# Performance work log

Hardware: AMD Instinct MI355X
Metric: run time of the kernel (lower is better)

Reference implementation:

```python
import jax, jax.numpy as jnp
import numpy as np

B, T, C, H = 4, 4096, 2048, 128  # batch, seq, emb_dim, head_size


def setup_inputs() -> dict:
    key = jax.random.key(0)
    k1, k2, k3, k4 = jax.random.split(key, 4)
    idx = jax.random.normal(k1, (B, T, C), dtype=jnp.float32)
    # nn.Linear weight layout: [out_features, in_features]; scale like torch init
    s = 1.0 / np.sqrt(C)
    Wq = jax.random.uniform(k2, (H, C), jnp.float32, -s, s)
    Wk = jax.random.uniform(k3, (H, C), jnp.float32, -s, s)
    Wv = jax.random.uniform(k4, (H, C), jnp.float32, -s, s)
    return {"idx": idx, "Wq": Wq, "Wk": Wk, "Wv": Wv}


def reference(idx, Wq, Wk, Wv):
    b, t, c = idx.shape
    q = jnp.einsum('btc,hc->bth', idx, Wq)  # [B,T,H]
    k = jnp.einsum('btc,hc->bth', idx, Wk)
    v = jnp.einsum('btc,hc->bth', idx, Wv)
    # NOTE: original computes keys @ queries^T and scales by emb_dim**-0.5
    scale = jnp.asarray(c, idx.dtype) ** -0.5
    wei = jnp.einsum('bih,bjh->bij', k, q) * scale  # [B,T,T]
    causal = jnp.tril(jnp.ones((t, t), dtype=bool))
    wei = jnp.where(causal, wei, -jnp.inf)
    wei = jax.nn.softmax(wei, axis=-1)
    return jnp.einsum('bij,bjh->bih', wei, v)  # [B,T,H]
```

## Files before the change

kernel.cpp:

```cpp
#include <hip/hip_runtime.h>
#include <hip/hip_bf16.h>
#include <cstdint>

#define TSEQ 4096
#define CDIM 2048
#define HDIM 128

typedef short bf8v __attribute__((ext_vector_type(8)));
typedef float f4v  __attribute__((ext_vector_type(4)));

__device__ __forceinline__ unsigned short f2b(float f) {
  union { float f; unsigned u; } v; v.f = f;
  unsigned u = v.u;
  return (unsigned short)((u + 0x7fffu + ((u >> 16) & 1u)) >> 16);
}

__device__ __forceinline__ f4v mfma16(bf8v a, bf8v b, f4v c) {
  return __builtin_amdgcn_mfma_f32_16x16x32_bf16(a, b, c, 0, 0, 0);
}

__global__ void wcat_kernel(const float* __restrict__ Wq, const float* __restrict__ Wk,
                            const float* __restrict__ Wv, unsigned short* __restrict__ Wcat) {
  int e = (blockIdx.x * 256 + threadIdx.x) * 4;
  int n = e >> 11;
  int k = e & 2047;
  const float* src;
  if (n < 128)      src = Wq + (size_t)n * CDIM + k;
  else if (n < 256) src = Wk + (size_t)(n - 128) * CDIM + k;
  else              src = Wv + (size_t)(n - 256) * CDIM + k;
  float4 f = *(const float4*)src;
  ushort4 o;
  o.x = f2b(f.x); o.y = f2b(f.y); o.z = f2b(f.z); o.w = f2b(f.w);
  *(ushort4*)(Wcat + e) = o;
}

__global__ __launch_bounds__(512, 6) void proj_gemm(const float* __restrict__ A,
                                                    const unsigned short* __restrict__ Bw,
                                                    unsigned short* __restrict__ QB,
                                                    unsigned short* __restrict__ KA,
                                                    unsigned short* __restrict__ VB) {
  __shared__ union {
    struct { unsigned short As[2][64][40]; unsigned short Bs[2][128][40]; } st;
    unsigned short Ct[64][132];
  } sm;
  const int m0 = blockIdx.x * 64;
  const int y  = blockIdx.y;
  const int n0 = y * 128;
  const int tid = threadIdx.x;
  const int lane = tid & 63;
  const int w = tid >> 6;
  const int wm = (w & 1) * 32, wn = (w >> 1) * 32;
  const int llo = lane & 15, lhi = lane >> 4;

  f4v acc[2][2];
#pragma unroll
  for (int i = 0; i < 2; ++i)
#pragma unroll
    for (int j = 0; j < 2; ++j) acc[i][j] = (f4v){0.f, 0.f, 0.f, 0.f};

  const int arow = tid >> 3, acol = (tid & 7) * 4;
  const int brow = tid >> 2, bcol = (tid & 3) * 8;
  const float* aptr = A + (size_t)(m0 + arow) * CDIM + acol;
  const unsigned short* bptr = Bw + (size_t)(n0 + brow) * CDIM + bcol;

  float4 fa = *(const float4*)(aptr);
  uint4  ub = *(const uint4*)(bptr);
  {
    ushort4 o;
    o.x = f2b(fa.x); o.y = f2b(fa.y); o.z = f2b(fa.z); o.w = f2b(fa.w);
    *(ushort4*)&sm.st.As[0][arow][acol] = o;
    *(uint4*)&sm.st.Bs[0][brow][bcol]   = ub;
  }

  for (int it = 0; it < 64; ++it) {
    const int cur = it & 1;
    __syncthreads();
    if (it < 63) {
      fa = *(const float4*)(aptr + (it + 1) * 32);
      ub = *(const uint4*)(bptr + (it + 1) * 32);
    }
    bf8v af[2], bfr[2];
    af[0]  = *(const bf8v*)&sm.st.As[cur][wm + llo][lhi * 8];
    af[1]  = *(const bf8v*)&sm.st.As[cur][wm + 16 + llo][lhi * 8];
    bfr[0] = *(const bf8v*)&sm.st.Bs[cur][wn + llo][lhi * 8];
    bfr[1] = *(const bf8v*)&sm.st.Bs[cur][wn + 16 + llo][lhi * 8];
#pragma unroll
    for (int i = 0; i < 2; ++i)
#pragma unroll
      for (int j = 0; j < 2; ++j) acc[i][j] = mfma16(af[i], bfr[j], acc[i][j]);
    if (it < 63) {
      ushort4 o;
      o.x = f2b(fa.x); o.y = f2b(fa.y); o.z = f2b(fa.z); o.w = f2b(fa.w);
      int nxt = cur ^ 1;
      *(ushort4*)&sm.st.As[nxt][arow][acol] = o;
      *(uint4*)&sm.st.Bs[nxt][brow][bcol]   = ub;
    }
  }
  __syncthreads();
#pragma unroll
  for (int i = 0; i < 2; ++i)
#pragma unroll
    for (int j = 0; j < 2; ++j)
#pragma unroll
      for (int r = 0; r < 4; ++r)
        sm.Ct[wm + i * 16 + lhi * 4 + r][wn + j * 16 + llo] = f2b(acc[i][j][r]);
  __syncthreads();
  if (y < 2) {
    unsigned short* dst = (y == 0) ? QB : KA;
    const size_t base16 = (size_t)(m0 >> 4);
#pragma unroll
    for (int p = 0; p < 2; ++p) {
      int g = p * 512 + tid;
      int t16l = g >> 8, kk = (g >> 6) & 3, ln = g & 63;
      int lo = ln & 15, hi = ln >> 4;
      bf8v v = *(const bf8v*)&sm.Ct[t16l * 16 + lo][kk * 32 + hi * 8];
      *(bf8v*)(dst + (((base16 + t16l) * 4 + kk) * 64 + ln) * 8) = v;
    }
  } else {
    const size_t base32 = (size_t)(m0 >> 5);
#pragma unroll
    for (int p = 0; p < 3; ++p) {
      int g = p * 512 + tid;
      if (g < 1152) {
        int jbl = g / 576;
        int ht  = (g % 576) >> 6;
        int ln  = g & 63;
        int lo = ln & 15, hi = ln >> 4;
        bf8v v;
        if (ht == 8) {
#pragma unroll
          for (int e = 0; e < 8; ++e) v[e] = (lo == 0) ? (short)0x3F80 : (short)0;
        } else {
#pragma unroll
          for (int e = 0; e < 8; ++e) v[e] = (short)sm.Ct[jbl * 32 + hi * 8 + e][ht * 16 + lo];
        }
        *(bf8v*)(VB + (((base32 + jbl) * 9 + ht) * 512 + (size_t)ln * 8)) = v;
      }
    }
  }
}

__global__ __launch_bounds__(256, 4) void attn6(const unsigned short* __restrict__ QB,
                                                const unsigned short* __restrict__ KA,
                                                const unsigned short* __restrict__ VB,
                                                float* __restrict__ out) {
  __shared__ union SM {
    unsigned short Ps[4][2][16][68];
    struct { float Om[4][16][68]; float Lm[4][16]; } mg;
  } sm;
  const int x = blockIdx.x;
  const int b = x & 3;
  const int u = x >> 2;
  const int g = u >> 6, r0 = u & 63;
  const int s = (g & 1) ? (g * 64 + 63 - r0) : (g * 64 + r0);
  const int lastjt = s >> 2;
  const int tid = threadIdx.x;
  const int w = tid >> 6, lane = tid & 63;
  const int llo = lane & 15, lhi = lane >> 4;
  const float scale = 0.022097086912079608f;

  bf8v aK[4];
  {
    const unsigned short* kp = KA + (size_t)(b * 256 + s) * 2048;
#pragma unroll
    for (int kk = 0; kk < 4; ++kk) aK[kk] = *(const bf8v*)(kp + (kk * 64 + lane) * 8);
  }

  f4v Oacc[9];
#pragma unroll
  for (int nt = 0; nt < 9; ++nt) Oacc[nt] = (f4v){0.f, 0.f, 0.f, 0.f};

  auto computeS = [&](int jtS, int buf) {
    const unsigned short* qp = QB + (size_t)(b * 256 + jtS * 4) * 2048;
#pragma unroll
    for (int ct = 0; ct < 4; ++ct) {
      f4v acc = (f4v){0.f, 0.f, 0.f, 0.f};
#pragma unroll
      for (int kk = 0; kk < 4; ++kk) {
        bf8v bq = *(const bf8v*)(qp + ((ct * 4 + kk) * 64 + lane) * 8);
        acc = mfma16(aK[kk], bq, acc);
      }
#pragma unroll
      for (int r = 0; r < 4; ++r) {
        float sv = acc[r];
        if (jtS == lastjt) {
          int j = jtS * 64 + ct * 16 + llo;
          int i = s * 16 + lhi * 4 + r;
          if (j > i) sv = -3.0e38f;
        }
        sm.Ps[w][buf][lhi * 4 + r][ct * 16 + llo] = f2b(__expf(sv * scale));
      }
    }
  };

  if (w <= lastjt) computeS(w, 0);
  int buf = 0;
  for (int jt = w; jt <= lastjt; jt += 4) {
    bf8v aP0 = *(const bf8v*)&sm.Ps[w][buf][llo][lhi * 8];
    bf8v aP1 = *(const bf8v*)&sm.Ps[w][buf][llo][32 + lhi * 8];
    if (jt + 4 <= lastjt) computeS(jt + 4, buf ^ 1);
    const unsigned short* vp = VB + (size_t)(b * 128 + jt * 2) * 4608;
#pragma unroll
    for (int nt = 0; nt < 9; ++nt) {
      f4v o = Oacc[nt];
      o = mfma16(aP0, *(const bf8v*)(vp + nt * 512 + (size_t)lane * 8), o);
      o = mfma16(aP1, *(const bf8v*)(vp + 4608 + nt * 512 + (size_t)lane * 8), o);
      Oacc[nt] = o;
    }
    buf ^= 1;
  }

#pragma unroll
  for (int half = 0; half < 2; ++half) {
    __syncthreads();
#pragma unroll
    for (int nt = 0; nt < 4; ++nt)
#pragma unroll
      for (int r = 0; r < 4; ++r)
        sm.mg.Om[w][lhi * 4 + r][nt * 16 + llo] = Oacc[half * 4 + nt][r];
    if (half == 0 && llo == 0) {
#pragma unroll
      for (int r = 0; r < 4; ++r) sm.mg.Lm[w][lhi * 4 + r] = Oacc[8][r];
    }
    __syncthreads();
    {
      int row = tid >> 4, c0 = (tid & 15) * 4;
      float L = sm.mg.Lm[0][row] + sm.mg.Lm[1][row] + sm.mg.Lm[2][row] + sm.mg.Lm[3][row];
      float inv = 1.0f / L;
      float* op = out + (size_t)(b * TSEQ + s * 16 + row) * HDIM + half * 64 + c0;
#pragma unroll
      for (int e = 0; e < 4; ++e) {
        float o = sm.mg.Om[0][row][c0 + e] + sm.mg.Om[1][row][c0 + e] +
                  sm.mg.Om[2][row][c0 + e] + sm.mg.Om[3][row][c0 + e];
        op[e] = o * inv;
      }
    }
  }
}

extern "C" void kernel_launch(void* const* d_in, const int* in_sizes, int n_in,
                              void* d_out, int out_size, void* d_ws, size_t ws_size,
                              hipStream_t stream) {
  const float* idx = (const float*)d_in[0];
  const float* Wq  = (const float*)d_in[1];
  const float* Wk  = (const float*)d_in[2];
  const float* Wv  = (const float*)d_in[3];
  float* out = (float*)d_out;
  char* ws = (char*)d_ws;
  unsigned short* Wcat = (unsigned short*)ws;
  unsigned short* QB   = (unsigned short*)(ws + ((size_t)2  << 20));
  unsigned short* KA   = (unsigned short*)(ws + ((size_t)7  << 20));
  unsigned short* VB   = (unsigned short*)(ws + ((size_t)12 << 20));

  wcat_kernel<<<768, 256, 0, stream>>>(Wq, Wk, Wv, Wcat);
  proj_gemm<<<dim3(256, 3), 512, 0, stream>>>(idx, Wcat, QB, KA, VB);
  attn6<<<1024, 256, 0, stream>>>(QB, KA, VB, out);
}
```

Baseline: 290.4 us.

## Pre-pack weights in MFMA fragment layout and load B directly into registers

The weight conversion kernel now writes bf16 weights already arranged in the MFMA fragment order, so the projection GEMM loads B operands straight from global memory into registers and skips LDS staging for B. The K step per iteration doubles to 64, halving the barrier count, and the A tile is stored in fragment order so each lane reads one contiguous 16-byte chunk. Launch bounds drop from 6 to 4 waves per SIMD to make room for the extra register buffers. The cost is higher register pressure and lower occupancy, and each wave pair rereads B from global or L2 instead of sharing it through LDS.

```diff
diff --git a/kernel.cpp b/kernel.cpp
--- a/kernel.cpp
+++ b/kernel.cpp
@@ -19,33 +19,36 @@
   return __builtin_amdgcn_mfma_f32_16x16x32_bf16(a, b, c, 0, 0, 0);
 }
 
-__global__ void wcat_kernel(const float* __restrict__ Wq, const float* __restrict__ Wk,
-                            const float* __restrict__ Wv, unsigned short* __restrict__ Wcat) {
-  int e = (blockIdx.x * 256 + threadIdx.x) * 4;
-  int n = e >> 11;
-  int k = e & 2047;
-  const float* src;
-  if (n < 128)      src = Wq + (size_t)n * CDIM + k;
-  else if (n < 256) src = Wk + (size_t)(n - 128) * CDIM + k;
-  else              src = Wv + (size_t)(n - 256) * CDIM + k;
-  float4 f = *(const float4*)src;
-  ushort4 o;
-  o.x = f2b(f.x); o.y = f2b(f.y); o.z = f2b(f.z); o.w = f2b(f.w);
-  *(ushort4*)(Wcat + e) = o;
-}
-
-__global__ __launch_bounds__(512, 6) void proj_gemm(const float* __restrict__ A,
-                                                    const unsigned short* __restrict__ Bw,
+__global__ void wcat_pack(const float* __restrict__ Wq, const float* __restrict__ Wk,
+                          const float* __restrict__ Wv, unsigned short* __restrict__ WB) {
+  int g = blockIdx.x * 256 + threadIdx.x;
+  int lane = g & 63, kk = (g >> 6) & 63, t24 = g >> 12;
+  int y = t24 >> 3, t16 = t24 & 7;
+  int row = t16 * 16 + (lane & 15);
+  int k   = kk * 32 + (lane >> 4) * 8;
+  const float* W = (y == 0) ? Wq : ((y == 1) ? Wk : Wv);
+  const float* src = W + (size_t)row * CDIM + k;
+  float4 f0 = *(const float4*)(src);
+  float4 f1 = *(const float4*)(src + 4);
+  ushort4 o0, o1;
+  o0.x = f2b(f0.x); o0.y = f2b(f0.y); o0.z = f2b(f0.z); o0.w = f2b(f0.w);
+  o1.x = f2b(f1.x); o1.y = f2b(f1.y); o1.z = f2b(f1.z); o1.w = f2b(f1.w);
+  unsigned short* d = WB + (size_t)g * 8;
+  *(ushort4*)(d)     = o0;
+  *(ushort4*)(d + 4) = o1;
+}
+
+__global__ __launch_bounds__(512, 4) void proj_gemm(const float* __restrict__ A,
+                                                    const unsigned short* __restrict__ WB,
                                                     unsigned short* __restrict__ QB,
                                                     unsigned short* __restrict__ KA,
                                                     unsigned short* __restrict__ VB) {
   __shared__ union {
-    struct { unsigned short As[2][64][40]; unsigned short Bs[2][128][40]; } st;
+    unsigned short As[2][512][8];
     unsigned short Ct[64][132];
   } sm;
   const int m0 = blockIdx.x * 64;
   const int y  = blockIdx.y;
-  const int n0 = y * 128;
   const int tid = threadIdx.x;
   const int lane = tid & 63;
   const int w = tid >> 6;
@@ -58,42 +61,60 @@
 #pragma unroll
     for (int j = 0; j < 2; ++j) acc[i][j] = (f4v){0.f, 0.f, 0.f, 0.f};
 
-  const int arow = tid >> 3, acol = (tid & 7) * 4;
-  const int brow = tid >> 2, bcol = (tid & 3) * 8;
-  const float* aptr = A + (size_t)(m0 + arow) * CDIM + acol;
-  const unsigned short* bptr = Bw + (size_t)(n0 + brow) * CDIM + bcol;
-
-  float4 fa = *(const float4*)(aptr);
-  uint4  ub = *(const uint4*)(bptr);
+  const int t16l = tid >> 7, kk2 = (tid >> 6) & 1;
+  const float* aptr = A + (size_t)(m0 + t16l * 16 + llo) * CDIM + kk2 * 32 + lhi * 8;
+  const unsigned short* wb0 = WB + (((size_t)(y * 8 + (w >> 1) * 2) * 64) * 64 + lane) * 8;
+  const unsigned short* wb1 = wb0 + (size_t)64 * 64 * 8;
+
+  float4 fa0 = *(const float4*)(aptr);
+  float4 fa1 = *(const float4*)(aptr + 4);
   {
-    ushort4 o;
-    o.x = f2b(fa.x); o.y = f2b(fa.y); o.z = f2b(fa.z); o.w = f2b(fa.w);
-    *(ushort4*)&sm.st.As[0][arow][acol] = o;
-    *(uint4*)&sm.st.Bs[0][brow][bcol]   = ub;
-  }
-
-  for (int it = 0; it < 64; ++it) {
+    ushort4 o0, o1;
+    o0.x = f2b(fa0.x); o0.y = f2b(fa0.y); o0.z = f2b(fa0.z); o0.w = f2b(fa0.w);
+    o1.x = f2b(fa1.x); o1.y = f2b(fa1.y); o1.z = f2b(fa1.z); o1.w = f2b(fa1.w);
+    *(ushort4*)&sm.As[0][tid][0] = o0;
+    *(ushort4*)&sm.As[0][tid][4] = o1;
+  }
+  bf8v bcur[4], bnxt[4];
+#pragma unroll
+  for (int ks = 0; ks < 2; ++ks) {
+    bcur[ks * 2 + 0] = *(const bf8v*)(wb0 + (size_t)ks * 512);
+    bcur[ks * 2 + 1] = *(const bf8v*)(wb1 + (size_t)ks * 512);
+  }
+
+  for (int it = 0; it < 32; ++it) {
     const int cur = it & 1;
     __syncthreads();
-    if (it < 63) {
-      fa = *(const float4*)(aptr + (it + 1) * 32);
-      ub = *(const uint4*)(bptr + (it + 1) * 32);
-    }
-    bf8v af[2], bfr[2];
-    af[0]  = *(const bf8v*)&sm.st.As[cur][wm + llo][lhi * 8];
-    af[1]  = *(const bf8v*)&sm.st.As[cur][wm + 16 + llo][lhi * 8];
-    bfr[0] = *(const bf8v*)&sm.st.Bs[cur][wn + llo][lhi * 8];
-    bfr[1] = *(const bf8v*)&sm.st.Bs[cur][wn + 16 + llo][lhi * 8];
+    if (it < 31) {
+      fa0 = *(const float4*)(aptr + (it + 1) * 64);
+      fa1 = *(const float4*)(aptr + (it + 1) * 64 + 4);
+#pragma unroll
+      for (int ks = 0; ks < 2; ++ks) {
+        bnxt[ks * 2 + 0] = *(const bf8v*)(wb0 + ((size_t)(it + 1) * 2 + ks) * 512);
+        bnxt[ks * 2 + 1] = *(const bf8v*)(wb1 + ((size_t)(it + 1) * 2 + ks) * 512);
+      }
+    }
+    bf8v af[2][2];
 #pragma unroll
     for (int i = 0; i < 2; ++i)
 #pragma unroll
-      for (int j = 0; j < 2; ++j) acc[i][j] = mfma16(af[i], bfr[j], acc[i][j]);
-    if (it < 63) {
-      ushort4 o;
-      o.x = f2b(fa.x); o.y = f2b(fa.y); o.z = f2b(fa.z); o.w = f2b(fa.w);
-      int nxt = cur ^ 1;
-      *(ushort4*)&sm.st.As[nxt][arow][acol] = o;
-      *(uint4*)&sm.st.Bs[nxt][brow][bcol]   = ub;
+      for (int ks = 0; ks < 2; ++ks)
+        af[i][ks] = *(const bf8v*)&sm.As[cur][(((w & 1) * 2 + i) * 2 + ks) * 64 + lane][0];
+#pragma unroll
+    for (int ks = 0; ks < 2; ++ks)
+#pragma unroll
+      for (int i = 0; i < 2; ++i)
+#pragma unroll
+        for (int j = 0; j < 2; ++j)
+          acc[i][j] = mfma16(af[i][ks], bcur[ks * 2 + j], acc[i][j]);
+    if (it < 31) {
+      ushort4 o0, o1;
+      o0.x = f2b(fa0.x); o0.y = f2b(fa0.y); o0.z = f2b(fa0.z); o0.w = f2b(fa0.w);
+      o1.x = f2b(fa1.x); o1.y = f2b(fa1.y); o1.z = f2b(fa1.z); o1.w = f2b(fa1.w);
+      *(ushort4*)&sm.As[cur ^ 1][tid][0] = o0;
+      *(ushort4*)&sm.As[cur ^ 1][tid][4] = o1;
+#pragma unroll
+      for (int q = 0; q < 4; ++q) bcur[q] = bnxt[q];
     }
   }
   __syncthreads();
@@ -111,10 +132,10 @@
 #pragma unroll
     for (int p = 0; p < 2; ++p) {
       int g = p * 512 + tid;
-      int t16l = g >> 8, kk = (g >> 6) & 3, ln = g & 63;
+      int t16g = g >> 8, kk = (g >> 6) & 3, ln = g & 63;
       int lo = ln & 15, hi = ln >> 4;
-      bf8v v = *(const bf8v*)&sm.Ct[t16l * 16 + lo][kk * 32 + hi * 8];
-      *(bf8v*)(dst + (((base16 + t16l) * 4 + kk) * 64 + ln) * 8) = v;
+      bf8v v = *(const bf8v*)&sm.Ct[t16g * 16 + lo][kk * 32 + hi * 8];
+      *(bf8v*)(dst + (((base16 + t16g) * 4 + kk) * 64 + ln) * 8) = v;
     }
   } else {
     const size_t base32 = (size_t)(m0 >> 5);
@@ -247,12 +268,12 @@
   const float* Wv  = (const float*)d_in[3];
   float* out = (float*)d_out;
   char* ws = (char*)d_ws;
-  unsigned short* Wcat = (unsigned short*)ws;
-  unsigned short* QB   = (unsigned short*)(ws + ((size_t)2  << 20));
-  unsigned short* KA   = (unsigned short*)(ws + ((size_t)7  << 20));
-  unsigned short* VB   = (unsigned short*)(ws + ((size_t)12 << 20));
-
-  wcat_kernel<<<768, 256, 0, stream>>>(Wq, Wk, Wv, Wcat);
-  proj_gemm<<<dim3(256, 3), 512, 0, stream>>>(idx, Wcat, QB, KA, VB);
+  unsigned short* WB = (unsigned short*)ws;
+  unsigned short* QB = (unsigned short*)(ws + ((size_t)2  << 20));
+  unsigned short* KA = (unsigned short*)(ws + ((size_t)7  << 20));
+  unsigned short* VB = (unsigned short*)(ws + ((size_t)12 << 20));
+
+  wcat_pack<<<384, 256, 0, stream>>>(Wq, Wk, Wv, WB);
+  proj_gemm<<<dim3(256, 3), 512, 0, stream>>>(idx, WB, QB, KA, VB);
   attn6<<<1024, 256, 0, stream>>>(QB, KA, VB, out);
 }
```

New measurement: 307.6 us. 5.9% more time.
